# Performance work log

Measured on AMD Instinct MI355X. Metric: run time of the kernel, lower is better.

The kernel has to match this reference:

```python
import jax, jax.numpy as jnp
import numpy as np
from jax import lax

NFEATS = 128
NMODES = 2
KH = KW = 3


def _conv_lstm_step(h, c, inp, W, b):
    """Standard ConvLSTMCell: conv over [inp, h] -> 4 gates -> c/h update.
    inp: (B, Cin, H, W); h, c: (B, nfeats, H, W); W: (4*nfeats, Cin+nfeats, 3, 3)."""
    z = lax.conv_general_dilated(
        jnp.concatenate([inp, h], axis=1), W,
        window_strides=(1, 1), padding='SAME',
        dimension_numbers=('NCHW', 'OIHW', 'NCHW'))
    z = z + b[None, :, None, None]
    i, f, o, g = jnp.split(z, 4, axis=1)
    c_next = jax.nn.sigmoid(f) * c + jax.nn.sigmoid(i) * jnp.tanh(g)
    h_next = jax.nn.sigmoid(o) * jnp.tanh(c_next)
    return h_next, c_next


def setup_inputs() -> dict:
    key = jax.random.key(0)
    ks = jax.random.split(key, 8)
    B, T, H, Wsp = 4, 8, 32, 32
    x1 = jax.random.normal(ks[0], (B, T, NFEATS, H, Wsp), dtype=jnp.float32)
    x2 = jax.random.normal(ks[1], (B, T, NFEATS, H, Wsp), dtype=jnp.float32)
    s = 0.02
    W1 = jax.random.normal(ks[2], (4 * NFEATS, NMODES * NFEATS + NFEATS, KH, KW), dtype=jnp.float32) * s
    b1 = jnp.zeros((4 * NFEATS,), dtype=jnp.float32)
    W2 = jax.random.normal(ks[3], (4 * NFEATS, 2 * NFEATS, KH, KW), dtype=jnp.float32) * s
    b2 = jnp.zeros((4 * NFEATS,), dtype=jnp.float32)
    W3 = jax.random.normal(ks[4], (4 * NFEATS, 2 * NFEATS, KH, KW), dtype=jnp.float32) * s
    b3 = jnp.zeros((4 * NFEATS,), dtype=jnp.float32)
    return {"x1": x1, "x2": x2, "W1": W1, "b1": b1, "W2": W2, "b2": b2, "W3": W3, "b3": b3}


def reference(x1, x2, W1, b1, W2, b2, W3, b3):
    # cat modalities on channel dim: (B, T, nmodes*nfeats, H, W)
    x = jnp.concatenate([x1, x2], axis=2)
    B, T, C, H, Wsp = x.shape
    zero = jnp.zeros((B, NFEATS, H, Wsp), dtype=x.dtype)
    carry0 = (zero, zero, zero, zero, zero, zero)  # h1,c1,h2,c2,h3,c3
    xs = jnp.moveaxis(x, 1, 0)  # (T, B, C, H, W)

    def step(carry, xt):
        h1, c1, h2, c2, h3, c3 = carry
        h1, c1 = _conv_lstm_step(h1, c1, xt, W1, b1)
        h2, c2 = _conv_lstm_step(h2, c2, h1, W2, b2)
        h3, c3 = _conv_lstm_step(h3, c3, h2, W3, b3)
        return (h1, c1, h2, c2, h3, c3), None

    (h1, c1, h2, c2, h3, c3), _ = lax.scan(step, carry0, xs)
    return h3
```

## Files before the change

### kernel.cpp

```cpp
#include <hip/hip_runtime.h>
#include <hip/hip_bf16.h>

typedef unsigned short u16;
typedef __attribute__((ext_vector_type(8))) short short8;
typedef __attribute__((ext_vector_type(4))) short short4v;
typedef __attribute__((ext_vector_type(4))) float floatx4;

__device__ __forceinline__ u16 f2bf(float x) {
  unsigned u = __float_as_uint(x);
  u += 0x7fffu + ((u >> 16) & 1u);
  return (u16)(u >> 16);
}
__device__ __forceinline__ float bf2f(u16 u) {
  return __uint_as_float(((unsigned)u) << 16);
}
__device__ __forceinline__ float sigm(float x) {
  return 1.0f / (1.0f + __expf(-x));
}


__global__ __launch_bounds__(256) void xsplit_kernel(
    const float* __restrict__ x1, const float* __restrict__ x2,
    u16* __restrict__ Xh, u16* __restrict__ Xl)
{
  __shared__ float lds[128][65];
  int bx  = blockIdx.x;
  int sel = bx >> 9;
  int rem = bx & 511;
  int bt  = rem >> 4;
  int pg  = rem & 15;
  int b = bt >> 3, t = bt & 7;
  int p0 = pg << 6;
  const float* src = (sel ? x2 : x1) + ((size_t)bt << 17);
  int tid = threadIdx.x;
  #pragma unroll
  for (int k2 = 0; k2 < 8; ++k2) {
    int idx = tid + (k2 << 8);
    int c = idx >> 4, p4 = (idx & 15) << 2;
    floatx4 v = *reinterpret_cast<const floatx4*>(src + ((size_t)c << 10) + p0 + p4);
    lds[c][p4] = v[0]; lds[c][p4 + 1] = v[1]; lds[c][p4 + 2] = v[2]; lds[c][p4 + 3] = v[3];
  }
  __syncthreads();
  int pl = tid >> 2;
  int cg = (tid & 3) << 5;
  size_t obase = (((size_t)((t * 4 + b) * 1024 + p0 + pl)) << 8) + (sel << 7) + cg;
  #pragma unroll
  for (int q = 0; q < 4; ++q) {
    short8 hv, lv;
    #pragma unroll
    for (int j = 0; j < 8; ++j) {
      float f = lds[cg + q * 8 + j][pl];
      u16 h = f2bf(f);
      hv[j] = (short)h;
      lv[j] = (short)f2bf(f - bf2f(h));
    }
    *reinterpret_cast<short8*>(Xh + obase + q * 8) = hv;
    *reinterpret_cast<short8*>(Xl + obase + q * 8) = lv;
  }
}

__global__ __launch_bounds__(256) void wsplit_kernel(
    const float* __restrict__ W, u16* __restrict__ Wh, u16* __restrict__ Wl, int CIN)
{
  int K = CIN * 9;
  int i = blockIdx.x * 256 + threadIdx.x;
  int np = i / K;
  int k = i - np * K;
  int e9 = k / CIN;
  int ci = k - e9 * CIN;
  int n = (np & 3) * 128 + (np >> 2);
  float v = W[((size_t)n * CIN + ci) * 9 + e9];
  size_t o = ((size_t)((np >> 4) * (K >> 3) + (k >> 3)) * 16 + (np & 15)) * 8 + (k & 7);
  u16 h = f2bf(v);
  Wh[o] = h;
  Wl[o] = f2bf(v - bf2f(h));
}

__global__ __launch_bounds__(256) void init_state(
    float* __restrict__ c1, float* __restrict__ c2, float* __restrict__ c3,
    u16* __restrict__ h1h, u16* __restrict__ h1l,
    u16* __restrict__ h2h, u16* __restrict__ h2l,
    u16* __restrict__ h3h, u16* __restrict__ h3l)
{
  int i = blockIdx.x * 256 + threadIdx.x;
  c1[i] = 0.f; c2[i] = 0.f; c3[i] = 0.f;
  h1h[i] = 0; h1l[i] = 0; h2h[i] = 0; h2l[i] = 0; h3h[i] = 0; h3l[i] = 0;
}

template<bool FUSE, int YR, int BPC, int DEPTH>
__global__ __launch_bounds__(256, BPC) void conv_gemm(
    const u16* __restrict__ A1h, const u16* __restrict__ A1l, int CA,
    const u16* __restrict__ A2h, const u16* __restrict__ A2l, int CB,
    const u16* __restrict__ Wh, const u16* __restrict__ Wl,
    int WCIN, int wcoff, int WK,
    float* __restrict__ zout,
    const float* __restrict__ zx,
    const float* __restrict__ bias,
    float* __restrict__ c, u16* __restrict__ hh, u16* __restrict__ hl,
    float* __restrict__ hout)
{
  constexpr int PROWS = (YR + 2) * 34;
  constexpr int HALOB = PROWS * 128;
  constexpr int MF = 2 * YR;
  constexpr int RLD = (PROWS * 8 + 255) / 256;
  const int CIN = CA + CB;

  __shared__ __align__(16) char smem[2 * HALOB];

  int tid = threadIdx.x;
  int bx  = blockIdx.x;
  int nt = (bx & 7) >> 1;
  int mt = ((bx >> 3) << 1) | (bx & 1);
  int m0 = mt * (32 * YR);
  int slot = m0 >> 10;
  int pbase = m0 & 1023;
  int y0 = pbase >> 5;
  int n0 = nt * 128;

  int lane = tid & 63, wid = tid >> 6;
  int nh = wid & 1, kh = wid >> 1;
  int fr = lane & 15, kq = lane >> 4;
  const int WK8 = WK >> 3;
  const int g16b = (n0 >> 4) + nh * 4;

  floatx4 acc[MF][4];
  #pragma unroll
  for (int i2 = 0; i2 < MF; ++i2)
    #pragma unroll
    for (int j2 = 0; j2 < 4; ++j2)
      acc[i2][j2] = (floatx4)0.0f;

  short8 RH[RLD], RL[RLD];
  const int NC = CIN >> 6;

  auto ldA = [&](int cc) {
    const u16 *sh, *sl; int cbase, CH;
    if (cc < CA) { sh = A1h; sl = A1l; cbase = cc;      CH = CA; }
    else         { sh = A2h; sl = A2l; cbase = cc - CA; CH = CB; }
    #pragma unroll
    for (int r = 0; r < RLD; ++r) {
      int u = tid + 256 * r;
      if (u < PROWS * 8) {
        int prow = u >> 3, cq = u & 7;
        int hrow = prow / 34;
        int xcol = prow - hrow * 34;
        int y = y0 - 1 + hrow;
        int x = xcol - 1;
        bool valid = ((unsigned)y < 32u) & ((unsigned)x < 32u);
        short8 vh = (short8)0, vl = (short8)0;
        if (valid) {
          size_t ab = (size_t)(slot * 1024 + y * 32 + x) * CH + cbase + cq * 8;
          vh = *reinterpret_cast<const short8*>(sh + ab);
          vl = *reinterpret_cast<const short8*>(sl + ab);
        }
        RH[r] = vh; RL[r] = vl;
      }
    }
  };

  auto stA = [&]() {
    #pragma unroll
    for (int r = 0; r < RLD; ++r) {
      int u = tid + 256 * r;
      if (u < PROWS * 8) {
        int prow = u >> 3, cq = u & 7;
        int off = prow * 128 + (((cq ^ (prow & 7)) & 7) << 4);
        *reinterpret_cast<short8*>(smem + off)         = RH[r];
        *reinterpret_cast<short8*>(smem + HALOB + off) = RL[r];
      }
    }
  };

  auto computeChunk = [&](int cc) {
    const int u0 = kh ? 9 : 0;
    short8 Bh_[9 + DEPTH][4], Bl_[9 + DEPTH][4];
    #pragma unroll
    for (int d = 0; d < DEPTH; ++d) {
      int kb = wcoff + ((u0 + d) >> 1) * WCIN + cc + ((u0 + d) & 1) * 32 + kq * 8;
      #pragma unroll
      for (int nf = 0; nf < 4; ++nf) {
        size_t bo = ((size_t)((g16b + nf) * WK8 + (kb >> 3)) * 16 + fr) * 8;
        Bh_[d][nf] = *reinterpret_cast<const short8*>(Wh + bo);
        Bl_[d][nf] = *reinterpret_cast<const short8*>(Wl + bo);
      }
    }
    #pragma unroll
    for (int ui = 0; ui < 9; ++ui) {
      if (ui + DEPTH < 9) {
        int un = u0 + ui + DEPTH;
        int kb = wcoff + (un >> 1) * WCIN + cc + (un & 1) * 32 + kq * 8;
        #pragma unroll
        for (int nf = 0; nf < 4; ++nf) {
          size_t bo = ((size_t)((g16b + nf) * WK8 + (kb >> 3)) * 16 + fr) * 8;
          Bh_[ui + DEPTH][nf] = *reinterpret_cast<const short8*>(Wh + bo);
          Bl_[ui + DEPTH][nf] = *reinterpret_cast<const short8*>(Wl + bo);
        }
      }
      int u = u0 + ui;
      int e9 = u >> 1, ks = u & 1;
      int dy = e9 / 3 - 1;
      int dx = e9 - (e9 / 3) * 3 - 1;
      short8 Ah_[MF], Al_[MF];
      #pragma unroll
      for (int mf = 0; mf < MF; ++mf) {
        int ar = mf * 16 + fr;
        int prow = ((ar >> 5) + 1 + dy) * 34 + (ar & 31) + 1 + dx;
        int off = prow * 128 + ((((ks * 4 + kq) ^ (prow & 7)) & 7) << 4);
        Ah_[mf] = *reinterpret_cast<const short8*>(smem + off);
        Al_[mf] = *reinterpret_cast<const short8*>(smem + HALOB + off);
      }
      __builtin_amdgcn_s_setprio(1);
      #pragma unroll
      for (int mf = 0; mf < MF; ++mf)
        #pragma unroll
        for (int nf = 0; nf < 4; ++nf)
          acc[mf][nf] = __builtin_amdgcn_mfma_f32_16x16x32_bf16(Ah_[mf], Bh_[ui][nf], acc[mf][nf], 0, 0, 0);
      #pragma unroll
      for (int mf = 0; mf < MF; ++mf)
        #pragma unroll
        for (int nf = 0; nf < 4; ++nf)
          acc[mf][nf] = __builtin_amdgcn_mfma_f32_16x16x32_bf16(Ah_[mf], Bl_[ui][nf], acc[mf][nf], 0, 0, 0);
      #pragma unroll
      for (int mf = 0; mf < MF; ++mf)
        #pragma unroll
        for (int nf = 0; nf < 4; ++nf)
          acc[mf][nf] = __builtin_amdgcn_mfma_f32_16x16x32_bf16(Al_[mf], Bh_[ui][nf], acc[mf][nf], 0, 0, 0);
      __builtin_amdgcn_s_setprio(0);
    }
  };

  ldA(0); stA();
  for (int q = 0; q < NC; ++q) {
    if (q + 1 < NC) ldA((q + 1) << 6);
    __syncthreads();
    computeChunk(q << 6);
    __syncthreads();
    if (q + 1 < NC) stA();
  }

  float (*tr)[68] = reinterpret_cast<float(*)[68]>(smem + nh * HALOB);
  if (kh == 0) {
    #pragma unroll
    for (int mf = 0; mf < MF; ++mf)
      #pragma unroll
      for (int nf = 0; nf < 4; ++nf)
        #pragma unroll
        for (int r = 0; r < 4; ++r)
          tr[mf * 16 + kq * 4 + r][nf * 16 + fr] = acc[mf][nf][r];
  }
  __syncthreads();
  if (kh == 1) {
    #pragma unroll
    for (int mf = 0; mf < MF; ++mf)
      #pragma unroll
      for (int nf = 0; nf < 4; ++nf)
        #pragma unroll
        for (int r = 0; r < 4; ++r)
          tr[mf * 16 + kq * 4 + r][nf * 16 + fr] += acc[mf][nf][r];
  }
  __syncthreads();

  int m  = (YR == 1) ? (lane & 31) : lane;
  int ol = (YR == 1) ? (lane >> 5) : 0;
  int ppix = pbase + m;
  size_t grow = (size_t)slot * 1024 + ppix;

  if (!FUSE) {
    size_t zrow = ((size_t)(m0 + m) << 9) + n0 + nh * 64 + kh * 32 + ol * 16;
    constexpr int NJ = (YR == 1) ? 4 : 8;
    #pragma unroll
    for (int j = 0; j < NJ; ++j) {
      floatx4 v = *reinterpret_cast<const floatx4*>(&tr[m][kh * 32 + ol * 16 + j * 4]);
      *reinterpret_cast<floatx4*>(zout + zrow + j * 4) = v;
    }
    return;
  }

  constexpr int NJ = (YR == 1) ? 4 : 8;
  int obc = kh * 8 + ol * 4;
  float cnv[NJ], hnv[NJ];
  #pragma unroll
  for (int j = 0; j < NJ; ++j) {
    int oc = obc + j;
    int ocg = nt * 32 + nh * 16 + oc;
    float zg[4];
    floatx4 tv = *reinterpret_cast<const floatx4*>(&tr[m][oc * 4]);
    if (zx) {
      floatx4 zv = *reinterpret_cast<const floatx4*>(zx + (grow << 9) + n0 + nh * 64 + oc * 4);
      #pragma unroll
      for (int g = 0; g < 4; ++g) zg[g] = tv[g] + zv[g] + bias[g * 128 + ocg];
    } else {
      #pragma unroll
      for (int g = 0; g < 4; ++g) zg[g] = tv[g] + bias[g * 128 + ocg];
    }
    size_t cidx = grow * 128 + ocg;
    float cvl = c[cidx];
    float cn = sigm(zg[1]) * cvl + sigm(zg[0]) * tanhf(zg[3]);
    float hn = sigm(zg[2]) * tanhf(cn);
    cnv[j] = cn; hnv[j] = hn;
    if (hout) hout[((size_t)slot * 128 + ocg) * 1024 + ppix] = hn;
  }
  size_t obase = grow * 128 + nt * 32 + nh * 16 + obc;
  if constexpr (YR == 1) {
    floatx4 cv; short4v hv, lv;
    #pragma unroll
    for (int j = 0; j < 4; ++j) {
      cv[j] = cnv[j];
      u16 hb = f2bf(hnv[j]);
      hv[j] = (short)hb;
      lv[j] = (short)f2bf(hnv[j] - bf2f(hb));
    }
    *reinterpret_cast<floatx4*>(c + obase) = cv;
    *reinterpret_cast<short4v*>(hh + obase) = hv;
    *reinterpret_cast<short4v*>(hl + obase) = lv;
  } else {
    floatx4 cv[2]; short8 hv, lv;
    #pragma unroll
    for (int j = 0; j < 8; ++j) {
      cv[j >> 2][j & 3] = cnv[j];
      u16 hb = f2bf(hnv[j]);
      hv[j] = (short)hb;
      lv[j] = (short)f2bf(hnv[j] - bf2f(hb));
    }
    *reinterpret_cast<floatx4*>(c + obase)     = cv[0];
    *reinterpret_cast<floatx4*>(c + obase + 4) = cv[1];
    *reinterpret_cast<short8*>(hh + obase) = hv;
    *reinterpret_cast<short8*>(hl + obase) = lv;
  }
}

extern "C" void kernel_launch(void* const* d_in, const int* in_sizes, int n_in,
                              void* d_out, int out_size, void* d_ws, size_t ws_size,
                              hipStream_t stream)
{
  const float* x1 = (const float*)d_in[0];
  const float* x2 = (const float*)d_in[1];
  const float* W1 = (const float*)d_in[2];
  const float* b1 = (const float*)d_in[3];
  const float* W2 = (const float*)d_in[4];
  const float* b2 = (const float*)d_in[5];
  const float* W3 = (const float*)d_in[6];
  const float* b3 = (const float*)d_in[7];
  float* out = (float*)d_out;

  char* ws = (char*)d_ws;
  size_t off = 0;
  auto alloc = [&](size_t bytes) {
    char* p = ws + off;
    off += (bytes + 255) & ~(size_t)255;
    return p;
  };
  u16*   Xh  = (u16*)  alloc(16777216);
  u16*   Xl  = (u16*)  alloc(16777216);
  u16*   W1h = (u16*)  alloc(3538944);
  u16*   W1l = (u16*)  alloc(3538944);
  u16*   W2h = (u16*)  alloc(2359296);
  u16*   W2l = (u16*)  alloc(2359296);
  u16*   W3h = (u16*)  alloc(2359296);
  u16*   W3l = (u16*)  alloc(2359296);
  u16*   hb_[12];
  for (int i = 0; i < 12; ++i) hb_[i] = (u16*)alloc(1048576);
  float* c1  = (float*)alloc(2097152);
  float* c2  = (float*)alloc(2097152);
  float* c3  = (float*)alloc(2097152);
  float* zx  = (float*)alloc(67108864);
  if (off > ws_size) return;

  u16 **h1h = &hb_[0], **h1l = &hb_[2], **h2h = &hb_[4], **h2l = &hb_[6],
      **h3h = &hb_[8], **h3l = &hb_[10];

  xsplit_kernel<<<1024, 256, 0, stream>>>(x1, x2, Xh, Xl);
  wsplit_kernel<<<6912, 256, 0, stream>>>(W1, W1h, W1l, 384);
  wsplit_kernel<<<4608, 256, 0, stream>>>(W2, W2h, W2l, 256);
  wsplit_kernel<<<4608, 256, 0, stream>>>(W3, W3h, W3l, 256);
  init_state<<<2048, 256, 0, stream>>>(c1, c2, c3,
      hb_[0], hb_[2], hb_[4], hb_[6], hb_[8], hb_[10]);

  conv_gemm<false, 2, 2, 1><<<2048, 256, 0, stream>>>(
      Xh, Xl, 256, nullptr, nullptr, 0, W1h, W1l, 384, 0, 3456,
      zx, nullptr, nullptr, nullptr, nullptr, nullptr, nullptr);

  for (int t = 0; t < 8; ++t) {
    int pi = t & 1, po = pi ^ 1;
    const float* zxt = zx + (size_t)t * 2097152;
    conv_gemm<true, 1, 2, 2><<<512, 256, 0, stream>>>(
        h1h[pi], h1l[pi], 128, nullptr, nullptr, 0, W1h, W1l, 384, 256, 3456,
        nullptr, zxt, b1, c1, h1h[po], h1l[po], nullptr);
    conv_gemm<true, 1, 2, 2><<<512, 256, 0, stream>>>(
        h1h[po], h1l[po], 128, h2h[pi], h2l[pi], 128, W2h, W2l, 256, 0, 2304,
        nullptr, nullptr, b2, c2, h2h[po], h2l[po], nullptr);
    conv_gemm<true, 1, 2, 2><<<512, 256, 0, stream>>>(
        h2h[po], h2l[po], 128, h3h[pi], h3l[pi], 128, W3h, W3l, 256, 0, 2304,
        nullptr, nullptr, b3, c3, h3h[po], h3l[po], (t == 7) ? out : nullptr);
  }
}
```

Baseline: 1.048 ms.

## Switch conv GEMM to 32x32x16 bf16 MFMA with 32-wide weight layout

Replaces the 16x16x32 MFMA tiling with 32x32x16 MFMA instructions. Each wave now holds 2 N-fragments of 32 columns and YR M-fragments of 32 rows, and the weight pre-split layout is regrouped into 32-row blocks to match. The block index decomposition into M/N tiles is simplified, and the accumulator transpose through shared memory is remapped to the 32x32 output lane layout. The aim is fewer LDS A-fragment loads per FLOP and higher MFMA throughput per instruction. The cost is longer-latency MFMA dependency chains on the same accumulators and a different register footprint.

```diff
diff --git a/kernel.cpp b/kernel.cpp
--- a/kernel.cpp
+++ b/kernel.cpp
@@ -5,6 +5,7 @@
 typedef __attribute__((ext_vector_type(8))) short short8;
 typedef __attribute__((ext_vector_type(4))) short short4v;
 typedef __attribute__((ext_vector_type(4))) float floatx4;
+typedef __attribute__((ext_vector_type(16))) float floatx16;
 
 __device__ __forceinline__ u16 f2bf(float x) {
   unsigned u = __float_as_uint(x);
@@ -70,7 +71,7 @@
   int ci = k - e9 * CIN;
   int n = (np & 3) * 128 + (np >> 2);
   float v = W[((size_t)n * CIN + ci) * 9 + e9];
-  size_t o = ((size_t)((np >> 4) * (K >> 3) + (k >> 3)) * 16 + (np & 15)) * 8 + (k & 7);
+  size_t o = ((size_t)((np >> 5) * (K >> 3) + (k >> 3)) * 32 + (np & 31)) * 8 + (k & 7);
   u16 h = f2bf(v);
   Wh[o] = h;
   Wl[o] = f2bf(v - bf2f(h));
@@ -101,7 +102,7 @@
 {
   constexpr int PROWS = (YR + 2) * 34;
   constexpr int HALOB = PROWS * 128;
-  constexpr int MF = 2 * YR;
+  constexpr int MF = YR;
   constexpr int RLD = (PROWS * 8 + 255) / 256;
   const int CIN = CA + CB;
 
@@ -109,8 +110,8 @@
 
   int tid = threadIdx.x;
   int bx  = blockIdx.x;
-  int nt = (bx & 7) >> 1;
-  int mt = ((bx >> 3) << 1) | (bx & 1);
+  int nt = bx & 3;
+  int mt = bx >> 2;
   int m0 = mt * (32 * YR);
   int slot = m0 >> 10;
   int pbase = m0 & 1023;
@@ -119,16 +120,16 @@
 
   int lane = tid & 63, wid = tid >> 6;
   int nh = wid & 1, kh = wid >> 1;
-  int fr = lane & 15, kq = lane >> 4;
+  int l31 = lane & 31, hl32 = lane >> 5;
   const int WK8 = WK >> 3;
-  const int g16b = (n0 >> 4) + nh * 4;
-
-  floatx4 acc[MF][4];
+  const int g32b = (n0 >> 5) + nh * 2;
+
+  floatx16 acc[MF][2];
   #pragma unroll
   for (int i2 = 0; i2 < MF; ++i2)
     #pragma unroll
-    for (int j2 = 0; j2 < 4; ++j2)
-      acc[i2][j2] = (floatx4)0.0f;
+    for (int j2 = 0; j2 < 2; ++j2)
+      acc[i2][j2] = (floatx16)0.0f;
 
   short8 RH[RLD], RL[RLD];
   const int NC = CIN >> 6;
@@ -173,59 +174,65 @@
 
   auto computeChunk = [&](int cc) {
     const int u0 = kh ? 9 : 0;
-    short8 Bh_[9 + DEPTH][4], Bl_[9 + DEPTH][4];
+    short8 Bh_[9 + DEPTH][2][2], Bl_[9 + DEPTH][2][2];
     #pragma unroll
     for (int d = 0; d < DEPTH; ++d) {
-      int kb = wcoff + ((u0 + d) >> 1) * WCIN + cc + ((u0 + d) & 1) * 32 + kq * 8;
-      #pragma unroll
-      for (int nf = 0; nf < 4; ++nf) {
-        size_t bo = ((size_t)((g16b + nf) * WK8 + (kb >> 3)) * 16 + fr) * 8;
-        Bh_[d][nf] = *reinterpret_cast<const short8*>(Wh + bo);
-        Bl_[d][nf] = *reinterpret_cast<const short8*>(Wl + bo);
+      int u = u0 + d;
+      #pragma unroll
+      for (int kstep = 0; kstep < 2; ++kstep) {
+        int k0 = wcoff + (u >> 1) * WCIN + cc + (u & 1) * 32 + kstep * 16;
+        int k8 = (k0 >> 3) + hl32;
+        #pragma unroll
+        for (int nf = 0; nf < 2; ++nf) {
+          size_t bo = ((size_t)((g32b + nf) * WK8 + k8) * 32 + l31) * 8;
+          Bh_[d][kstep][nf] = *reinterpret_cast<const short8*>(Wh + bo);
+          Bl_[d][kstep][nf] = *reinterpret_cast<const short8*>(Wl + bo);
+        }
       }
     }
     #pragma unroll
     for (int ui = 0; ui < 9; ++ui) {
       if (ui + DEPTH < 9) {
         int un = u0 + ui + DEPTH;
-        int kb = wcoff + (un >> 1) * WCIN + cc + (un & 1) * 32 + kq * 8;
-        #pragma unroll
-        for (int nf = 0; nf < 4; ++nf) {
-          size_t bo = ((size_t)((g16b + nf) * WK8 + (kb >> 3)) * 16 + fr) * 8;
-          Bh_[ui + DEPTH][nf] = *reinterpret_cast<const short8*>(Wh + bo);
-          Bl_[ui + DEPTH][nf] = *reinterpret_cast<const short8*>(Wl + bo);
+        #pragma unroll
+        for (int kstep = 0; kstep < 2; ++kstep) {
+          int k0 = wcoff + (un >> 1) * WCIN + cc + (un & 1) * 32 + kstep * 16;
+          int k8 = (k0 >> 3) + hl32;
+          #pragma unroll
+          for (int nf = 0; nf < 2; ++nf) {
+            size_t bo = ((size_t)((g32b + nf) * WK8 + k8) * 32 + l31) * 8;
+            Bh_[ui + DEPTH][kstep][nf] = *reinterpret_cast<const short8*>(Wh + bo);
+            Bl_[ui + DEPTH][kstep][nf] = *reinterpret_cast<const short8*>(Wl + bo);
+          }
         }
       }
       int u = u0 + ui;
-      int e9 = u >> 1, ks = u & 1;
+      int e9 = u >> 1, ks32 = u & 1;
       int dy = e9 / 3 - 1;
       int dx = e9 - (e9 / 3) * 3 - 1;
-      short8 Ah_[MF], Al_[MF];
-      #pragma unroll
-      for (int mf = 0; mf < MF; ++mf) {
-        int ar = mf * 16 + fr;
-        int prow = ((ar >> 5) + 1 + dy) * 34 + (ar & 31) + 1 + dx;
-        int off = prow * 128 + ((((ks * 4 + kq) ^ (prow & 7)) & 7) << 4);
-        Ah_[mf] = *reinterpret_cast<const short8*>(smem + off);
-        Al_[mf] = *reinterpret_cast<const short8*>(smem + HALOB + off);
+      #pragma unroll
+      for (int kstep = 0; kstep < 2; ++kstep) {
+        int cq = ks32 * 4 + kstep * 2 + hl32;
+        short8 Ah_[MF], Al_[MF];
+        #pragma unroll
+        for (int mf = 0; mf < MF; ++mf) {
+          int ar = mf * 32 + l31;
+          int prow = ((ar >> 5) + 1 + dy) * 34 + (ar & 31) + 1 + dx;
+          int off = prow * 128 + (((cq ^ (prow & 7)) & 7) << 4);
+          Ah_[mf] = *reinterpret_cast<const short8*>(smem + off);
+          Al_[mf] = *reinterpret_cast<const short8*>(smem + HALOB + off);
+        }
+        __builtin_amdgcn_s_setprio(1);
+        #pragma unroll
+        for (int mf = 0; mf < MF; ++mf)
+          #pragma unroll
+          for (int nf = 0; nf < 2; ++nf) {
+            acc[mf][nf] = __builtin_amdgcn_mfma_f32_32x32x16_bf16(Ah_[mf], Bh_[ui][kstep][nf], acc[mf][nf], 0, 0, 0);
+            acc[mf][nf] = __builtin_amdgcn_mfma_f32_32x32x16_bf16(Ah_[mf], Bl_[ui][kstep][nf], acc[mf][nf], 0, 0, 0);
+            acc[mf][nf] = __builtin_amdgcn_mfma_f32_32x32x16_bf16(Al_[mf], Bh_[ui][kstep][nf], acc[mf][nf], 0, 0, 0);
+          }
+        __builtin_amdgcn_s_setprio(0);
       }
-      __builtin_amdgcn_s_setprio(1);
-      #pragma unroll
-      for (int mf = 0; mf < MF; ++mf)
-        #pragma unroll
-        for (int nf = 0; nf < 4; ++nf)
-          acc[mf][nf] = __builtin_amdgcn_mfma_f32_16x16x32_bf16(Ah_[mf], Bh_[ui][nf], acc[mf][nf], 0, 0, 0);
-      #pragma unroll
-      for (int mf = 0; mf < MF; ++mf)
-        #pragma unroll
-        for (int nf = 0; nf < 4; ++nf)
-          acc[mf][nf] = __builtin_amdgcn_mfma_f32_16x16x32_bf16(Ah_[mf], Bl_[ui][nf], acc[mf][nf], 0, 0, 0);
-      #pragma unroll
-      for (int mf = 0; mf < MF; ++mf)
-        #pragma unroll
-        for (int nf = 0; nf < 4; ++nf)
-          acc[mf][nf] = __builtin_amdgcn_mfma_f32_16x16x32_bf16(Al_[mf], Bh_[ui][nf], acc[mf][nf], 0, 0, 0);
-      __builtin_amdgcn_s_setprio(0);
     }
   };
 
@@ -238,25 +245,25 @@
     if (q + 1 < NC) stA();
   }
 
-  float (*tr)[68] = reinterpret_cast<float(*)[68]>(smem + nh * HALOB);
+  float (*tr)[68] = reinterpret_cast<float(*)[68]>(smem + nh * (YR == 1 ? 8704 : 17408));
   if (kh == 0) {
     #pragma unroll
     for (int mf = 0; mf < MF; ++mf)
       #pragma unroll
-      for (int nf = 0; nf < 4; ++nf)
-        #pragma unroll
-        for (int r = 0; r < 4; ++r)
-          tr[mf * 16 + kq * 4 + r][nf * 16 + fr] = acc[mf][nf][r];
+      for (int nf = 0; nf < 2; ++nf)
+        #pragma unroll
+        for (int r = 0; r < 16; ++r)
+          tr[mf * 32 + (r & 3) + 8 * (r >> 2) + 4 * hl32][nf * 32 + l31] = acc[mf][nf][r];
   }
   __syncthreads();
   if (kh == 1) {
     #pragma unroll
     for (int mf = 0; mf < MF; ++mf)
       #pragma unroll
-      for (int nf = 0; nf < 4; ++nf)
-        #pragma unroll
-        for (int r = 0; r < 4; ++r)
-          tr[mf * 16 + kq * 4 + r][nf * 16 + fr] += acc[mf][nf][r];
+      for (int nf = 0; nf < 2; ++nf)
+        #pragma unroll
+        for (int r = 0; r < 16; ++r)
+          tr[mf * 32 + (r & 3) + 8 * (r >> 2) + 4 * hl32][nf * 32 + l31] += acc[mf][nf][r];
   }
   __syncthreads();
 
```

After: 1.132 ms. +8.0%, slower.
